# Performance work log

Measured on AMD Instinct MI355X. Metric: run time of the kernel, lower is better.

Reference implementation:

```python
import jax, jax.numpy as jnp
import numpy as np

TAU = 10.0  # matches init kwarg


def setup_inputs() -> dict:
    key = jax.random.key(0)
    k1, k2, k3 = jax.random.split(key, 3)
    B, E, L, V = 4, 512, 512, 32000
    embed_EN = jax.random.normal(k1, (B, E, L), dtype=jnp.float32)
    embed_DE = jax.random.normal(k2, (B, E, L), dtype=jnp.float32)
    embed_M = jax.random.normal(k3, (V, E), dtype=jnp.float32)
    return {"embed_EN": embed_EN, "embed_DE": embed_DE, "embed_M": embed_M}


def reference(embed_EN, embed_DE, embed_M):
    inv_tau = 1.0 / TAU
    # distance: [B, L, V] = (embed_DE^T [B,L,E]) @ embed_M^T [E,V]
    distance = jnp.einsum('bel,ve->blv', embed_DE, embed_M)
    # up: [B, L] numerator, dot over embed dim
    up = jnp.exp(inv_tau * jnp.sum(embed_EN * embed_DE, axis=1))
    # down: [B, L] softmax-style denominator over vocab
    down = jnp.sum(jnp.exp(inv_tau * distance), axis=2)
    return jnp.sum(up / down)
```

## Files before the change

### kernel.cpp

```cpp
#include <hip/hip_runtime.h>

using f16   = _Float16;
using f16x4 = __attribute__((ext_vector_type(4))) _Float16;
using f16x8 = __attribute__((ext_vector_type(8))) _Float16;
using f32x4 = __attribute__((ext_vector_type(4))) float;

#define BDIM 4
#define EDIM 512
#define LDIM 512
#define VDIM 32000
#define RDIM 2048
#define INV_TAU 0.1f

using gcvoid = const __attribute__((address_space(1))) void;
using lvoid  = __attribute__((address_space(3))) void;

__device__ __forceinline__ void gload_lds16(const void* g, void* l) {
  __builtin_amdgcn_global_load_lds((gcvoid*)g, (lvoid*)l, 16, 0, 0);
}

__global__ void cvtA_kernel(const float* __restrict__ DE, f16* __restrict__ A16) {
  __shared__ float tile[64][65];
  const int b  = blockIdx.z;
  const int e0 = blockIdx.y * 64;
  const int l0 = blockIdx.x * 64;
  const int t  = threadIdx.x;
#pragma unroll
  for (int i = 0; i < 4; ++i) {
    int idx = t + i * 256;
    int el  = idx >> 4;
    int l4  = (idx & 15) * 4;
    float4 v = *reinterpret_cast<const float4*>(
        DE + (size_t)(b * 512 + e0 + el) * 512 + l0 + l4);
    tile[el][l4 + 0] = v.x;
    tile[el][l4 + 1] = v.y;
    tile[el][l4 + 2] = v.z;
    tile[el][l4 + 3] = v.w;
  }
  __syncthreads();
#pragma unroll
  for (int i = 0; i < 4; ++i) {
    int idx = t + i * 256;
    int ll  = idx >> 4;
    int e4  = (idx & 15) * 4;
    f16x4 h;
    h[0] = (f16)tile[e4 + 0][ll];
    h[1] = (f16)tile[e4 + 1][ll];
    h[2] = (f16)tile[e4 + 2][ll];
    h[3] = (f16)tile[e4 + 3][ll];
    *reinterpret_cast<f16x4*>(A16 + (size_t)(b * 512 + l0 + ll) * 512 + e0 + e4) = h;
  }
}

__global__ void cvtM_kernel(const float* __restrict__ M, f16* __restrict__ B16) {
  const size_t N4 = (size_t)VDIM * EDIM / 4;
  const size_t stride = (size_t)gridDim.x * blockDim.x;
  for (size_t i = (size_t)blockIdx.x * blockDim.x + threadIdx.x; i < N4; i += stride) {
    float4 v = reinterpret_cast<const float4*>(M)[i];
    f16x4 h = { (f16)v.x, (f16)v.y, (f16)v.z, (f16)v.w };
    reinterpret_cast<f16x4*>(B16)[i] = h;
  }
}

__global__ __launch_bounds__(256, 2) void gemm_kernel(const f16* __restrict__ A16,
                                                      const f16* __restrict__ B16,
                                                      float* __restrict__ down) {
  __shared__ __align__(16) char sm[4][16384];
  const int orig = blockIdx.x;
  const int bid  = (orig & 7) * 500 + (orig >> 3);
  const int rt   = bid & 15;
  const int ct   = bid >> 4;
  const int r0   = rt * 128, c0 = ct * 128;
  const int tid  = threadIdx.x;
  const int lane = tid & 63;
  const int w    = tid >> 6;
  const int wr   = w >> 1, wc = w & 1;

  const int srow = lane >> 2;
  const int sel  = ((lane & 3) ^ ((lane >> 3) & 3)) * 8;

  auto stage = [&](int buf, int t) {
    const int kbase = t * 32;
#pragma unroll
    for (int i = 0; i < 2; ++i) {
      int instr = w * 2 + i;
      gload_lds16(A16 + (size_t)(r0 + instr * 16 + srow) * 512 + kbase + sel,
                  &sm[buf][instr * 1024]);
    }
#pragma unroll
    for (int i = 0; i < 2; ++i) {
      int instr = w * 2 + i;
      gload_lds16(B16 + (size_t)(c0 + instr * 16 + srow) * 512 + kbase + sel,
                  &sm[buf][8192 + instr * 1024]);
    }
  };

  f32x4 acc[4][4] = {};

  stage(0, 0);
  stage(1, 1);
  stage(2, 2);
  asm volatile("s_waitcnt vmcnt(8)" ::: "memory");
  __builtin_amdgcn_s_barrier();
  asm volatile("" ::: "memory");

  const int koff = (((lane >> 4) ^ ((lane >> 1) & 3)) * 16);
  const int arow = (wr * 64 + (lane & 15)) * 64;
  const int brow = (wc * 64 + (lane & 15)) * 64;

#pragma unroll
  for (int t = 0; t < 16; ++t) {
    const int cur = t & 3;
    f16x8 af[4], bf[4];
#pragma unroll
    for (int mi = 0; mi < 4; ++mi)
      af[mi] = *reinterpret_cast<const f16x8*>(&sm[cur][arow + mi * 1024 + koff]);
#pragma unroll
    for (int ni = 0; ni < 4; ++ni)
      bf[ni] = *reinterpret_cast<const f16x8*>(&sm[cur][8192 + brow + ni * 1024 + koff]);

    if (t + 3 < 16) stage((t + 3) & 3, t + 3);

    __builtin_amdgcn_s_setprio(1);
#pragma unroll
    for (int mi = 0; mi < 4; ++mi)
#pragma unroll
      for (int ni = 0; ni < 4; ++ni)
        acc[mi][ni] = __builtin_amdgcn_mfma_f32_16x16x32_f16(
            af[mi], bf[ni], acc[mi][ni], 0, 0, 0);
    __builtin_amdgcn_s_setprio(0);

    if (t < 15) {
      if (t <= 12)      asm volatile("s_waitcnt vmcnt(8) lgkmcnt(0)" ::: "memory");
      else if (t == 13) asm volatile("s_waitcnt vmcnt(4) lgkmcnt(0)" ::: "memory");
      else              asm volatile("s_waitcnt vmcnt(0) lgkmcnt(0)" ::: "memory");
      __builtin_amdgcn_s_barrier();
      asm volatile("" ::: "memory");
    }
  }

  const int rbase = r0 + wr * 64;
#pragma unroll
  for (int mi = 0; mi < 4; ++mi) {
    float s0 = 0.f, s1 = 0.f, s2 = 0.f, s3 = 0.f;
#pragma unroll
    for (int ni = 0; ni < 4; ++ni) {
      f32x4 v = acc[mi][ni];
      s0 += __expf(INV_TAU * v[0]);
      s1 += __expf(INV_TAU * v[1]);
      s2 += __expf(INV_TAU * v[2]);
      s3 += __expf(INV_TAU * v[3]);
    }
#pragma unroll
    for (int m = 1; m <= 8; m <<= 1) {
      s0 += __shfl_xor(s0, m);
      s1 += __shfl_xor(s1, m);
      s2 += __shfl_xor(s2, m);
      s3 += __shfl_xor(s3, m);
    }
    if ((lane & 15) == 0) {
      int row = rbase + mi * 16 + (lane >> 4) * 4;
      atomicAdd(&down[row + 0], s0);
      atomicAdd(&down[row + 1], s1);
      atomicAdd(&down[row + 2], s2);
      atomicAdd(&down[row + 3], s3);
    }
  }
}

__global__ void finalize_kernel(const float* __restrict__ EN, const float* __restrict__ DE,
                                const float* __restrict__ down, float* __restrict__ out) {
  __shared__ float red[4][64];
  const int r0 = blockIdx.x * 64;
  const int b  = r0 >> 9;
  const int l0 = r0 & 511;
  const int t  = threadIdx.x;
  const int ll = t & 63;
  const int g  = t >> 6;
  float p = 0.f;
  const int ebase = g * 128;
#pragma unroll 4
  for (int e = 0; e < 128; ++e) {
    size_t idx = (size_t)(b * 512 + ebase + e) * 512 + l0 + ll;
    p += EN[idx] * DE[idx];
  }
  red[g][ll] = p;
  __syncthreads();
  if (t < 64) {
    float s = red[0][t] + red[1][t] + red[2][t] + red[3][t];
    float val = __expf(INV_TAU * s) / down[r0 + t];
#pragma unroll
    for (int m = 1; m <= 32; m <<= 1) val += __shfl_xor(val, m);
    if (t == 0) atomicAdd(out, val);
  }
}

extern "C" void kernel_launch(void* const* d_in, const int* in_sizes, int n_in,
                              void* d_out, int out_size, void* d_ws, size_t ws_size,
                              hipStream_t stream) {
  const float* EN = (const float*)d_in[0];
  const float* DE = (const float*)d_in[1];
  const float* M  = (const float*)d_in[2];

  float* down = (float*)d_ws;
  f16* A16 = (f16*)((char*)d_ws + 8192);
  f16* B16 = (f16*)((char*)d_ws + 8192 + (size_t)RDIM * EDIM * 2);
  const size_t need = 8192 + (size_t)RDIM * EDIM * 2 + (size_t)VDIM * EDIM * 2;

  hipMemsetAsync(d_out, 0, sizeof(float), stream);
  if (ws_size < need) return;
  hipMemsetAsync(d_ws, 0, RDIM * sizeof(float), stream);

  cvtA_kernel<<<dim3(8, 8, 4), 256, 0, stream>>>(DE, A16);
  cvtM_kernel<<<2048, 256, 0, stream>>>(M, B16);
  gemm_kernel<<<4000, 256, 0, stream>>>(A16, B16, down);
  finalize_kernel<<<32, 256, 0, stream>>>(EN, DE, down, (float*)d_out);
}
```

Before: 125.1 us.

## Use three-stage LDS pipeline for occupancy and split EN·DE dot over more blocks

The GEMM cuts its LDS ring buffer from four stages to three, so each block uses 48KB instead of 64KB, and raises launch bounds to three blocks per CU. The aim is more resident waves to hide latency, at the cost of one less stage of prefetch lookahead. The finalize step is also split: a new 256-block kernel computes the EN·DE dot products with atomics into a partial buffer, and a small kernel applies the exp and divide and does the final reduction. This replaces a 32-block kernel that did a serial 128-step loop per thread.

```diff
diff --git a/kernel.cpp b/kernel.cpp
--- a/kernel.cpp
+++ b/kernel.cpp
@@ -62,10 +62,10 @@
   }
 }
 
-__global__ __launch_bounds__(256, 2) void gemm_kernel(const f16* __restrict__ A16,
+__global__ __launch_bounds__(256, 3) void gemm_kernel(const f16* __restrict__ A16,
                                                       const f16* __restrict__ B16,
                                                       float* __restrict__ down) {
-  __shared__ __align__(16) char sm[4][16384];
+  __shared__ __align__(16) char sm[3][16384];
   const int orig = blockIdx.x;
   const int bid  = (orig & 7) * 500 + (orig >> 3);
   const int rt   = bid & 15;
@@ -99,8 +99,7 @@
 
   stage(0, 0);
   stage(1, 1);
-  stage(2, 2);
-  asm volatile("s_waitcnt vmcnt(8)" ::: "memory");
+  asm volatile("s_waitcnt vmcnt(4)" ::: "memory");
   __builtin_amdgcn_s_barrier();
   asm volatile("" ::: "memory");
 
@@ -110,7 +109,7 @@
 
 #pragma unroll
   for (int t = 0; t < 16; ++t) {
-    const int cur = t & 3;
+    const int cur = t % 3;
     f16x8 af[4], bf[4];
 #pragma unroll
     for (int mi = 0; mi < 4; ++mi)
@@ -119,7 +118,7 @@
     for (int ni = 0; ni < 4; ++ni)
       bf[ni] = *reinterpret_cast<const f16x8*>(&sm[cur][8192 + brow + ni * 1024 + koff]);
 
-    if (t + 3 < 16) stage((t + 3) & 3, t + 3);
+    if (t + 2 < 16) stage((t + 2) % 3, t + 2);
 
     __builtin_amdgcn_s_setprio(1);
 #pragma unroll
@@ -131,9 +130,8 @@
     __builtin_amdgcn_s_setprio(0);
 
     if (t < 15) {
-      if (t <= 12)      asm volatile("s_waitcnt vmcnt(8) lgkmcnt(0)" ::: "memory");
-      else if (t == 13) asm volatile("s_waitcnt vmcnt(4) lgkmcnt(0)" ::: "memory");
-      else              asm volatile("s_waitcnt vmcnt(0) lgkmcnt(0)" ::: "memory");
+      if (t <= 13) asm volatile("s_waitcnt vmcnt(4) lgkmcnt(0)" ::: "memory");
+      else         asm volatile("s_waitcnt vmcnt(0) lgkmcnt(0)" ::: "memory");
       __builtin_amdgcn_s_barrier();
       asm volatile("" ::: "memory");
     }
@@ -168,19 +166,21 @@
   }
 }
 
-__global__ void finalize_kernel(const float* __restrict__ EN, const float* __restrict__ DE,
-                                const float* __restrict__ down, float* __restrict__ out) {
+__global__ void partial_kernel(const float* __restrict__ EN, const float* __restrict__ DE,
+                               float* __restrict__ partial) {
   __shared__ float red[4][64];
-  const int r0 = blockIdx.x * 64;
+  const int bk = blockIdx.x;
+  const int r0 = (bk & 31) * 64;
+  const int eo = (bk >> 5) * 64;
   const int b  = r0 >> 9;
   const int l0 = r0 & 511;
   const int t  = threadIdx.x;
   const int ll = t & 63;
   const int g  = t >> 6;
   float p = 0.f;
-  const int ebase = g * 128;
+  const int ebase = eo + g * 16;
 #pragma unroll 4
-  for (int e = 0; e < 128; ++e) {
+  for (int e = 0; e < 16; ++e) {
     size_t idx = (size_t)(b * 512 + ebase + e) * 512 + l0 + ll;
     p += EN[idx] * DE[idx];
   }
@@ -188,11 +188,24 @@
   __syncthreads();
   if (t < 64) {
     float s = red[0][t] + red[1][t] + red[2][t] + red[3][t];
-    float val = __expf(INV_TAU * s) / down[r0 + t];
-#pragma unroll
-    for (int m = 1; m <= 32; m <<= 1) val += __shfl_xor(val, m);
-    if (t == 0) atomicAdd(out, val);
-  }
+    atomicAdd(&partial[r0 + t], s);
+  }
+}
+
+__global__ void finalize2_kernel(const float* __restrict__ partial,
+                                 const float* __restrict__ down,
+                                 float* __restrict__ out) {
+  __shared__ float red[4];
+  const int r = blockIdx.x * 256 + threadIdx.x;
+  const int lane = threadIdx.x & 63;
+  const int w = threadIdx.x >> 6;
+  float val = __expf(INV_TAU * partial[r]) / down[r];
+#pragma unroll
+  for (int m = 1; m <= 32; m <<= 1) val += __shfl_xor(val, m);
+  if (lane == 0) red[w] = val;
+  __syncthreads();
+  if (threadIdx.x == 0)
+    atomicAdd(out, red[0] + red[1] + red[2] + red[3]);
 }
 
 extern "C" void kernel_launch(void* const* d_in, const int* in_sizes, int n_in,
@@ -202,17 +215,19 @@
   const float* DE = (const float*)d_in[1];
   const float* M  = (const float*)d_in[2];
 
-  float* down = (float*)d_ws;
-  f16* A16 = (f16*)((char*)d_ws + 8192);
-  f16* B16 = (f16*)((char*)d_ws + 8192 + (size_t)RDIM * EDIM * 2);
-  const size_t need = 8192 + (size_t)RDIM * EDIM * 2 + (size_t)VDIM * EDIM * 2;
+  float* down    = (float*)d_ws;
+  float* partial = (float*)((char*)d_ws + 8192);
+  f16* A16 = (f16*)((char*)d_ws + 16384);
+  f16* B16 = (f16*)((char*)d_ws + 16384 + (size_t)RDIM * EDIM * 2);
+  const size_t need = 16384 + (size_t)RDIM * EDIM * 2 + (size_t)VDIM * EDIM * 2;
 
   hipMemsetAsync(d_out, 0, sizeof(float), stream);
   if (ws_size < need) return;
-  hipMemsetAsync(d_ws, 0, RDIM * sizeof(float), stream);
+  hipMemsetAsync(d_ws, 0, 16384, stream);
 
   cvtA_kernel<<<dim3(8, 8, 4), 256, 0, stream>>>(DE, A16);
   cvtM_kernel<<<2048, 256, 0, stream>>>(M, B16);
+  partial_kernel<<<256, 256, 0, stream>>>(EN, DE, partial);
   gemm_kernel<<<4000, 256, 0, stream>>>(A16, B16, down);
-  finalize_kernel<<<32, 256, 0, stream>>>(EN, DE, down, (float*)d_out);
-}
+  finalize2_kernel<<<8, 256, 0, stream>>>(partial, down, (float*)d_out);
+}
```

Result: faster. 120.2 us (-3.9%).
